# Performance work log

Measured on AMD Instinct MI355X. Metric: run time of the kernel, lower is better.

Reference implementation:

```python
import jax, jax.numpy as jnp
import numpy as np

EMBED = 8   # forced: combine_heads Linear(embed_dim, embed_dim) applied to 8-wire measurement
FFN = 32
B, S = 128, 8192
EPS = 1e-5


def _layernorm(x, g, b):
    m = x.mean(-1, keepdims=True)
    v = ((x - m) ** 2).mean(-1, keepdims=True)
    return (x - m) * jax.lax.rsqrt(v + EPS) * g + b


def setup_inputs() -> dict:
    key = jax.random.key(0)
    ks = jax.random.split(key, 8)

    def lin(k, fi, fo):
        return jax.random.normal(k, (fi, fo), jnp.float32) / np.sqrt(fi).astype(np.float32)

    return dict(
        x=jax.random.normal(ks[0], (B, S, EMBED), jnp.float32),
        Wq=lin(ks[1], EMBED, EMBED), bq=jnp.zeros((EMBED,), jnp.float32),
        theta_attn=jax.random.uniform(ks[2], (EMBED,), jnp.float32, -np.pi, np.pi),
        Wc=lin(ks[3], EMBED, EMBED), bc=jnp.zeros((EMBED,), jnp.float32),
        g1=jnp.ones((EMBED,), jnp.float32), beta1=jnp.zeros((EMBED,), jnp.float32),
        theta_ffn=jax.random.uniform(ks[4], (EMBED,), jnp.float32, -np.pi, np.pi),
        W1=lin(ks[5], EMBED, FFN), b1=jnp.zeros((FFN,), jnp.float32),
        W2=lin(ks[6], FFN, EMBED), b2=jnp.zeros((EMBED,), jnp.float32),
        g2=jnp.ones((EMBED,), jnp.float32), beta2=jnp.zeros((EMBED,), jnp.float32),
    )


def reference(x, Wq, bq, theta_attn, Wc, bc, g1, beta1,
              theta_ffn, W1, b1, W2, b2, g2, beta2):
    # --- MultiHeadAttentionQuantum (eval mode, dropout = identity) ---
    # q_linear; the 8-wire encoder consumes all 8 features of q per token.
    q = x @ Wq + bq                           # [B, S, 8]
    # Circuit per token: RX(q_i) then trainable RX(theta_i) on wire i -> RX(q_i+theta_i),
    # then CNOT ring (0->1,...,6->7, 7->0), then <Z_i>.
    # All-RX product state => basis probs p_i(1)=sin^2(a_i/2); CNOTs permute basis
    # states (prefix-XOR of bits), so analytically:
    #   <Z_k> = prod_{j=0..k} cos(a_j)  for k>=1;   <Z_0> = prod_{j=1..7} cos(a_j)
    ca = jnp.cos(q + theta_attn)              # [B, S, 8]
    z_rest = jnp.cumprod(ca, axis=-1)[..., 1:]
    z0 = jnp.prod(ca[..., 1:], axis=-1, keepdims=True)
    z = jnp.concatenate([z0, z_rest], axis=-1)
    attn_out = z @ Wc + bc                    # combine_heads

    x1 = _layernorm(x + attn_out, g1, beta1)

    # --- FeedForwardQuantum: RX(x_i) then RY(theta_i), no entanglers ->
    #     <Z_i> = cos(theta_i) * cos(x_i)  (product state, per-wire closed form)
    zf = jnp.cos(theta_ffn) * jnp.cos(x1)     # [B, S, 8]
    h = jax.nn.relu(zf @ W1 + b1)             # linear1 -> relu
    ffn_out = h @ W2 + b2                     # linear2

    return _layernorm(x1 + ffn_out, g2, beta2)
```

## Files before the change

### kernel.cpp

```cpp
#include <hip/hip_runtime.h>


#define NTOK   (128 * 8192)
#define NTHREADS 256
#define NBLOCKS  (NTOK / NTHREADS)
#define LN_EPS 1e-5f
#define INV2PI 0.15915494309189535f

typedef __fp16 half2_t __attribute__((ext_vector_type(2)));
typedef __fp16 half8_t __attribute__((ext_vector_type(8)));
typedef float  float4_t __attribute__((ext_vector_type(4)));

union PK  { unsigned u; half2_t h; };
union U4H { uint4 u; half8_t h; half2_t h2[4]; };

__device__ __forceinline__ float fast_cos_rev(float xrev) {
    return __builtin_amdgcn_cosf(xrev);
}
__device__ __forceinline__ float fast_cos(float x) {
    return __builtin_amdgcn_cosf(x * INV2PI);
}
__device__ __forceinline__ float fast_rsqrt(float x) {
    return __builtin_amdgcn_rsqf(x);
}
__device__ __forceinline__ unsigned packh2(float a, float b) {
    PK c; c.h = __builtin_amdgcn_cvt_pkrtz(a, b); return c.u;
}
__device__ __forceinline__ float dot2(half2_t a, unsigned bw, float c) {
    PK b; b.u = bw;
    return __builtin_amdgcn_fdot2(a, b.h, c, false);
}

__global__ void pack_weights(const float* __restrict__ Wq,
                             const float* __restrict__ W1,
                             const float* __restrict__ W2,
                             const float* __restrict__ Wc,
                             const float* __restrict__ bq,
                             const float* __restrict__ tha,
                             const float* __restrict__ thf,
                             unsigned* __restrict__ ws)
{
    int idx = threadIdx.x;
    if (idx < 32) {
        int k = idx >> 2, p = idx & 3;
        ws[idx] = packh2(Wq[(2 * p) * 8 + k] * INV2PI, Wq[(2 * p + 1) * 8 + k] * INV2PI);
    } else if (idx < 64) {
        int i2 = idx - 32;
        int kp = i2 >> 3, j = i2 & 7;
        ws[idx] = packh2(Wc[(2 * kp) * 8 + j], Wc[(2 * kp + 1) * 8 + j]);
    } else if (idx < 72) {
        int k = idx - 64;
        ws[idx] = __float_as_uint((bq[k] + tha[k]) * INV2PI);
    } else if (idx < 80) {
        int j = idx - 72;
        ws[idx] = __float_as_uint(__builtin_amdgcn_cosf(thf[j] * INV2PI));
    } else if (idx >= 128 && idx < 320) {
        int t  = (idx - 128) & 63;
        int tb = (idx - 128) >> 6;
        int n0 = t & 15, q = t >> 4;
        uint4 w = make_uint4(0u, 0u, 0u, 0u);
        unsigned r[4] = {0u, 0u, 0u, 0u};
        if (tb == 0) {
            if (q == 0)
                for (int p = 0; p < 4; ++p)
                    r[p] = packh2(W1[(2 * p) * 32 + n0], W1[(2 * p + 1) * 32 + n0]);
        } else if (tb == 1) {
            if (q == 0)
                for (int p = 0; p < 4; ++p)
                    r[p] = packh2(W1[(2 * p) * 32 + n0 + 16], W1[(2 * p + 1) * 32 + n0 + 16]);
        } else {
            if (n0 < 8)
                for (int p = 0; p < 4; ++p)
                    r[p] = packh2(W2[(8 * q + 2 * p) * 8 + n0], W2[(8 * q + 2 * p + 1) * 8 + n0]);
        }
        w.x = r[0]; w.y = r[1]; w.z = r[2]; w.w = r[3];
        reinterpret_cast<uint4*>(ws)[32 + tb * 64 + t] = w;
    }
}

__global__ __launch_bounds__(NTHREADS, 8)
void qtb_kernel(const float* __restrict__ x,
                const float* __restrict__ bc,
                const float* __restrict__ g1,  const float* __restrict__ be1,
                const float* __restrict__ b1,
                const float* __restrict__ b2,
                const float* __restrict__ g2,  const float* __restrict__ be2,
                const unsigned* __restrict__ wp,
                float* __restrict__ out)
{
    const int tid  = threadIdx.x;
    const int wave = tid >> 6;
    const int lane = tid & 63;
    const int col  = lane & 15;
    const int quad = lane >> 4;
    const int g    = blockIdx.x * NTHREADS + tid;

    const float4* px = reinterpret_cast<const float4*>(x) + (size_t)g * 2;
    float4 xa = px[0];
    float4 xb = px[1];

    const float* qb = reinterpret_cast<const float*>(wp + 64);
    const float* cf = reinterpret_cast<const float*>(wp + 72);

    __shared__ uint4    zbuf[4][64];
    __shared__ unsigned hbuf[4][16 * 20];
    __shared__ float    fbuf[4][64 * 9];

    const uint4* fr = reinterpret_cast<const uint4*>(wp);
    U4H B1a, B1b, B2;
    B1a.u = fr[32 + lane];
    B1b.u = fr[96 + lane];
    B2.u  = fr[160 + lane];
    const float b1a_s = b1[col];
    const float b1b_s = b1[col + 16];
    const float b2_s  = (col < 8) ? b2[col & 7] : 0.f;

    float xv[8];
    half2_t xp[4];
    xv[0] = xa.x; xv[1] = xa.y; xv[2] = xa.z; xv[3] = xa.w;
    xv[4] = xb.x; xv[5] = xb.y; xv[6] = xb.z; xv[7] = xb.w;
    xp[0] = __builtin_amdgcn_cvt_pkrtz(xa.x, xa.y);
    xp[1] = __builtin_amdgcn_cvt_pkrtz(xa.z, xa.w);
    xp[2] = __builtin_amdgcn_cvt_pkrtz(xb.x, xb.y);
    xp[3] = __builtin_amdgcn_cvt_pkrtz(xb.z, xb.w);

    float ca[8];
#pragma unroll
    for (int k = 0; k < 8; ++k) {
        float q = qb[k];
#pragma unroll
        for (int p = 0; p < 4; ++p) q = dot2(xp[p], wp[k * 4 + p], q);
        ca[k] = fast_cos_rev(q);
    }
    float attn[8];
#pragma unroll
    for (int j = 0; j < 8; ++j) attn[j] = bc[j];
    {
        float z[8];
        float cp  = ca[0];
        float cp1 = 1.0f;
#pragma unroll
        for (int k = 1; k < 8; ++k) {
            cp  *= ca[k];
            cp1 *= ca[k];
            z[k] = cp;
        }
        z[0] = cp1;
        half2_t zp[4];
#pragma unroll
        for (int p = 0; p < 4; ++p)
            zp[p] = __builtin_amdgcn_cvt_pkrtz(z[2 * p], z[2 * p + 1]);
#pragma unroll
        for (int p = 0; p < 4; ++p)
#pragma unroll
            for (int j = 0; j < 8; ++j)
                attn[j] = dot2(zp[p], wp[32 + p * 8 + j], attn[j]);
    }

    {
        float y[8];
        float s = 0.f;
#pragma unroll
        for (int j = 0; j < 8; ++j) { y[j] = xv[j] + attn[j]; s += y[j]; }
        float m = s * 0.125f;
        float v = 0.f;
#pragma unroll
        for (int j = 0; j < 8; ++j) { float d = y[j] - m; v += d * d; }
        float r = fast_rsqrt(v * 0.125f + LN_EPS);
        float zf[8];
#pragma unroll
        for (int j = 0; j < 8; ++j) {
            float x1 = (y[j] - m) * r * g1[j] + be1[j];
            xv[j] = x1;
            zf[j] = cf[j] * fast_cos(x1);
        }
        U4H zpk;
#pragma unroll
        for (int p = 0; p < 4; ++p)
            zpk.h2[p] = __builtin_amdgcn_cvt_pkrtz(zf[2 * p], zf[2 * p + 1]);
        zbuf[wave][lane] = zpk.u;
    }

    const unsigned psel = (quad < 2) ? 0x05040100u : 0x07060302u;
#pragma unroll
    for (int grp = 0; grp < 4; ++grp) {
        U4H A1; A1.u = zbuf[wave][grp * 16 + col];
        float4_t c1a = {b1a_s, b1a_s, b1a_s, b1a_s};
        float4_t c1b = {b1b_s, b1b_s, b1b_s, b1b_s};
        float4_t h0 = __builtin_amdgcn_mfma_f32_16x16x32_f16(A1.h, B1a.h, c1a, 0, 0, 0);
        float4_t h1 = __builtin_amdgcn_mfma_f32_16x16x32_f16(A1.h, B1b.h, c1b, 0, 0, 0);
#pragma unroll
        for (int r = 0; r < 4; ++r)
            hbuf[wave][(4 * quad + r) * 20 + col] =
                packh2(fmaxf(h0[r], 0.f), fmaxf(h1[r], 0.f));
        int hb = col * 20 + (quad & 1) * 8;
        uint4 w0 = *reinterpret_cast<const uint4*>(&hbuf[wave][hb]);
        uint4 w1 = *reinterpret_cast<const uint4*>(&hbuf[wave][hb + 4]);
        U4H A2;
        A2.u.x = __builtin_amdgcn_perm(w0.y, w0.x, psel);
        A2.u.y = __builtin_amdgcn_perm(w0.w, w0.z, psel);
        A2.u.z = __builtin_amdgcn_perm(w1.y, w1.x, psel);
        A2.u.w = __builtin_amdgcn_perm(w1.w, w1.z, psel);
        float4_t c2 = {b2_s, b2_s, b2_s, b2_s};
        float4_t f = __builtin_amdgcn_mfma_f32_16x16x32_f16(A2.h, B2.h, c2, 0, 0, 0);
        if (col < 8) {
#pragma unroll
            for (int r = 0; r < 4; ++r)
                fbuf[wave][(grp * 16 + 4 * quad + r) * 9 + col] = f[r];
        }
    }

    {
        float y[8];
        float s = 0.f;
#pragma unroll
        for (int j = 0; j < 8; ++j) {
            y[j] = xv[j] + fbuf[wave][lane * 9 + j];
            s += y[j];
        }
        float m = s * 0.125f;
        float v = 0.f;
#pragma unroll
        for (int j = 0; j < 8; ++j) { float d = y[j] - m; v += d * d; }
        float r = fast_rsqrt(v * 0.125f + LN_EPS);
        float o[8];
#pragma unroll
        for (int j = 0; j < 8; ++j) o[j] = (y[j] - m) * r * g2[j] + be2[j];
        float4* q = reinterpret_cast<float4*>(out) + (size_t)g * 2;
        q[0] = make_float4(o[0], o[1], o[2], o[3]);
        q[1] = make_float4(o[4], o[5], o[6], o[7]);
    }
}

extern "C" void kernel_launch(void* const* d_in, const int* in_sizes, int n_in,
                              void* d_out, int out_size, void* d_ws, size_t ws_size,
                              hipStream_t stream) {
    (void)in_sizes; (void)n_in; (void)ws_size; (void)out_size;
    unsigned* wp = (unsigned*)d_ws;
    pack_weights<<<1, 320, 0, stream>>>(
        (const float*)d_in[1],
        (const float*)d_in[9],
        (const float*)d_in[11],
        (const float*)d_in[4],
        (const float*)d_in[2],
        (const float*)d_in[3],
        (const float*)d_in[8],
        wp);
    qtb_kernel<<<NBLOCKS, NTHREADS, 0, stream>>>(
        (const float*)d_in[0],
        (const float*)d_in[5],
        (const float*)d_in[6],
        (const float*)d_in[7],
        (const float*)d_in[10],
        (const float*)d_in[12],
        (const float*)d_in[13],
        (const float*)d_in[14],
        wp,
        (float*)d_out);
}
```

Baseline: 113.4 us.

## Replace second FFN MFMA with per-thread fdot2 over full hidden row

```diff
diff --git a/kernel.cpp b/kernel.cpp
--- a/kernel.cpp
+++ b/kernel.cpp
@@ -12,7 +12,7 @@
 typedef float  float4_t __attribute__((ext_vector_type(4)));
 
 union PK  { unsigned u; half2_t h; };
-union U4H { uint4 u; half8_t h; half2_t h2[4]; };
+union U4H { uint4 u; half8_t h; half2_t h2[4]; unsigned w[4]; };
 
 __device__ __forceinline__ float fast_cos_rev(float xrev) {
     return __builtin_amdgcn_cosf(xrev);
@@ -54,31 +54,24 @@
     } else if (idx < 80) {
         int j = idx - 72;
         ws[idx] = __float_as_uint(__builtin_amdgcn_cosf(thf[j] * INV2PI));
-    } else if (idx >= 128 && idx < 320) {
-        int t  = (idx - 128) & 63;
-        int tb = (idx - 128) >> 6;
-        int n0 = t & 15, q = t >> 4;
-        uint4 w = make_uint4(0u, 0u, 0u, 0u);
+    } else if (idx < 208) {
+        int i2 = idx - 80;
+        int c = i2 >> 3, j = i2 & 7;
+        ws[idx] = packh2(W2[c * 8 + j], W2[(c + 16) * 8 + j]);
+    } else if (idx >= 256 && idx < 384) {
+        int t  = (idx - 256) & 63;
+        int tb = (idx - 256) >> 6;
+        int n0 = (t & 15) + tb * 16, q = t >> 4;
         unsigned r[4] = {0u, 0u, 0u, 0u};
-        if (tb == 0) {
-            if (q == 0)
-                for (int p = 0; p < 4; ++p)
-                    r[p] = packh2(W1[(2 * p) * 32 + n0], W1[(2 * p + 1) * 32 + n0]);
-        } else if (tb == 1) {
-            if (q == 0)
-                for (int p = 0; p < 4; ++p)
-                    r[p] = packh2(W1[(2 * p) * 32 + n0 + 16], W1[(2 * p + 1) * 32 + n0 + 16]);
-        } else {
-            if (n0 < 8)
-                for (int p = 0; p < 4; ++p)
-                    r[p] = packh2(W2[(8 * q + 2 * p) * 8 + n0], W2[(8 * q + 2 * p + 1) * 8 + n0]);
-        }
-        w.x = r[0]; w.y = r[1]; w.z = r[2]; w.w = r[3];
-        reinterpret_cast<uint4*>(ws)[32 + tb * 64 + t] = w;
-    }
-}
-
-__global__ __launch_bounds__(NTHREADS, 8)
+        if (q == 0)
+            for (int p = 0; p < 4; ++p)
+                r[p] = packh2(W1[(2 * p) * 32 + n0], W1[(2 * p + 1) * 32 + n0]);
+        uint4 w; w.x = r[0]; w.y = r[1]; w.z = r[2]; w.w = r[3];
+        reinterpret_cast<uint4*>(ws)[64 + tb * 64 + t] = w;
+    }
+}
+
+__global__ __launch_bounds__(NTHREADS, 6)
 void qtb_kernel(const float* __restrict__ x,
                 const float* __restrict__ bc,
                 const float* __restrict__ g1,  const float* __restrict__ be1,
@@ -103,17 +96,14 @@
     const float* cf = reinterpret_cast<const float*>(wp + 72);
 
     __shared__ uint4    zbuf[4][64];
-    __shared__ unsigned hbuf[4][16 * 20];
-    __shared__ float    fbuf[4][64 * 9];
+    __shared__ unsigned hbuf[4][64 * 20];
 
     const uint4* fr = reinterpret_cast<const uint4*>(wp);
-    U4H B1a, B1b, B2;
-    B1a.u = fr[32 + lane];
-    B1b.u = fr[96 + lane];
-    B2.u  = fr[160 + lane];
+    U4H B1a, B1b;
+    B1a.u = fr[64 + lane];
+    B1b.u = fr[128 + lane];
     const float b1a_s = b1[col];
     const float b1b_s = b1[col + 16];
-    const float b2_s  = (col < 8) ? b2[col & 7] : 0.f;
 
     float xv[8];
     half2_t xp[4];
@@ -181,7 +171,6 @@
         zbuf[wave][lane] = zpk.u;
     }
 
-    const unsigned psel = (quad < 2) ? 0x05040100u : 0x07060302u;
 #pragma unroll
     for (int grp = 0; grp < 4; ++grp) {
         U4H A1; A1.u = zbuf[wave][grp * 16 + col];
@@ -191,33 +180,33 @@
         float4_t h1 = __builtin_amdgcn_mfma_f32_16x16x32_f16(A1.h, B1b.h, c1b, 0, 0, 0);
 #pragma unroll
         for (int r = 0; r < 4; ++r)
-            hbuf[wave][(4 * quad + r) * 20 + col] =
+            hbuf[wave][(grp * 16 + 4 * quad + r) * 20 + col] =
                 packh2(fmaxf(h0[r], 0.f), fmaxf(h1[r], 0.f));
-        int hb = col * 20 + (quad & 1) * 8;
-        uint4 w0 = *reinterpret_cast<const uint4*>(&hbuf[wave][hb]);
-        uint4 w1 = *reinterpret_cast<const uint4*>(&hbuf[wave][hb + 4]);
-        U4H A2;
-        A2.u.x = __builtin_amdgcn_perm(w0.y, w0.x, psel);
-        A2.u.y = __builtin_amdgcn_perm(w0.w, w0.z, psel);
-        A2.u.z = __builtin_amdgcn_perm(w1.y, w1.x, psel);
-        A2.u.w = __builtin_amdgcn_perm(w1.w, w1.z, psel);
-        float4_t c2 = {b2_s, b2_s, b2_s, b2_s};
-        float4_t f = __builtin_amdgcn_mfma_f32_16x16x32_f16(A2.h, B2.h, c2, 0, 0, 0);
-        if (col < 8) {
-#pragma unroll
-            for (int r = 0; r < 4; ++r)
-                fbuf[wave][(grp * 16 + 4 * quad + r) * 9 + col] = f[r];
-        }
+    }
+
+    U4H hw[4];
+    {
+        const unsigned* hrow = &hbuf[wave][lane * 20];
+#pragma unroll
+        for (int c4 = 0; c4 < 4; ++c4)
+            hw[c4].u = *reinterpret_cast<const uint4*>(hrow + 4 * c4);
+    }
+    float ffn[8];
+#pragma unroll
+    for (int j = 0; j < 8; ++j) ffn[j] = b2[j];
+#pragma unroll
+    for (int c = 0; c < 16; ++c) {
+        half2_t hp = hw[c >> 2].h2[c & 3];
+#pragma unroll
+        for (int j = 0; j < 8; ++j)
+            ffn[j] = dot2(hp, wp[80 + c * 8 + j], ffn[j]);
     }
 
     {
         float y[8];
         float s = 0.f;
 #pragma unroll
-        for (int j = 0; j < 8; ++j) {
-            y[j] = xv[j] + fbuf[wave][lane * 9 + j];
-            s += y[j];
-        }
+        for (int j = 0; j < 8; ++j) { y[j] = xv[j] + ffn[j]; s += y[j]; }
         float m = s * 0.125f;
         float v = 0.f;
 #pragma unroll
@@ -237,7 +226,7 @@
                               hipStream_t stream) {
     (void)in_sizes; (void)n_in; (void)ws_size; (void)out_size;
     unsigned* wp = (unsigned*)d_ws;
-    pack_weights<<<1, 320, 0, stream>>>(
+    pack_weights<<<1, 384, 0, stream>>>(
         (const float*)d_in[1],
         (const float*)d_in[9],
         (const float*)d_in[11],
```

New measurement: 117.9 us. 3.9% more time.

## Use persistent blocks with grid-stride loop and register prefetch of next tokens

Applied to the files above, without the earlier changes.

```diff
diff --git a/kernel.cpp b/kernel.cpp
--- a/kernel.cpp
+++ b/kernel.cpp
@@ -1,9 +1,11 @@
 #include <hip/hip_runtime.h>
 
 
-#define NTOK   (128 * 8192)
+#define NTOK    (128 * 8192)
 #define NTHREADS 256
-#define NBLOCKS  (NTOK / NTHREADS)
+#define PBLOCKS 1024
+#define ITERS   4
+#define CHUNK   (PBLOCKS * NTHREADS)
 #define LN_EPS 1e-5f
 #define INV2PI 0.15915494309189535f
 
@@ -12,7 +14,7 @@
 typedef float  float4_t __attribute__((ext_vector_type(4)));
 
 union PK  { unsigned u; half2_t h; };
-union U4H { uint4 u; half8_t h; half2_t h2[4]; };
+union U4H { uint4 u; half8_t h; half2_t h2[4]; unsigned w[4]; };
 
 __device__ __forceinline__ float fast_cos_rev(float xrev) {
     return __builtin_amdgcn_cosf(xrev);
@@ -58,7 +60,6 @@
         int t  = (idx - 128) & 63;
         int tb = (idx - 128) >> 6;
         int n0 = t & 15, q = t >> 4;
-        uint4 w = make_uint4(0u, 0u, 0u, 0u);
         unsigned r[4] = {0u, 0u, 0u, 0u};
         if (tb == 0) {
             if (q == 0)
@@ -73,12 +74,12 @@
                 for (int p = 0; p < 4; ++p)
                     r[p] = packh2(W2[(8 * q + 2 * p) * 8 + n0], W2[(8 * q + 2 * p + 1) * 8 + n0]);
         }
-        w.x = r[0]; w.y = r[1]; w.z = r[2]; w.w = r[3];
+        uint4 w; w.x = r[0]; w.y = r[1]; w.z = r[2]; w.w = r[3];
         reinterpret_cast<uint4*>(ws)[32 + tb * 64 + t] = w;
     }
 }
 
-__global__ __launch_bounds__(NTHREADS, 8)
+__global__ __launch_bounds__(NTHREADS, 4)
 void qtb_kernel(const float* __restrict__ x,
                 const float* __restrict__ bc,
                 const float* __restrict__ g1,  const float* __restrict__ be1,
@@ -93,18 +94,13 @@
     const int lane = tid & 63;
     const int col  = lane & 15;
     const int quad = lane >> 4;
-    const int g    = blockIdx.x * NTHREADS + tid;
-
-    const float4* px = reinterpret_cast<const float4*>(x) + (size_t)g * 2;
-    float4 xa = px[0];
-    float4 xb = px[1];
 
     const float* qb = reinterpret_cast<const float*>(wp + 64);
     const float* cf = reinterpret_cast<const float*>(wp + 72);
 
     __shared__ uint4    zbuf[4][64];
     __shared__ unsigned hbuf[4][16 * 20];
-    __shared__ float    fbuf[4][64 * 9];
+    __shared__ float    fbuf[4][64 * 10];
 
     const uint4* fr = reinterpret_cast<const uint4*>(wp);
     U4H B1a, B1b, B2;
@@ -114,121 +110,142 @@
     const float b1a_s = b1[col];
     const float b1b_s = b1[col + 16];
     const float b2_s  = (col < 8) ? b2[col & 7] : 0.f;
-
-    float xv[8];
-    half2_t xp[4];
-    xv[0] = xa.x; xv[1] = xa.y; xv[2] = xa.z; xv[3] = xa.w;
-    xv[4] = xb.x; xv[5] = xb.y; xv[6] = xb.z; xv[7] = xb.w;
-    xp[0] = __builtin_amdgcn_cvt_pkrtz(xa.x, xa.y);
-    xp[1] = __builtin_amdgcn_cvt_pkrtz(xa.z, xa.w);
-    xp[2] = __builtin_amdgcn_cvt_pkrtz(xb.x, xb.y);
-    xp[3] = __builtin_amdgcn_cvt_pkrtz(xb.z, xb.w);
-
-    float ca[8];
-#pragma unroll
-    for (int k = 0; k < 8; ++k) {
-        float q = qb[k];
-#pragma unroll
-        for (int p = 0; p < 4; ++p) q = dot2(xp[p], wp[k * 4 + p], q);
-        ca[k] = fast_cos_rev(q);
+    const unsigned psel = (quad < 2) ? 0x05040100u : 0x07060302u;
+
+    size_t g = (size_t)blockIdx.x * NTHREADS + tid;
+    float4 nxa, nxb;
+    {
+        const float4* px = reinterpret_cast<const float4*>(x) + g * 2;
+        nxa = px[0]; nxb = px[1];
     }
-    float attn[8];
-#pragma unroll
-    for (int j = 0; j < 8; ++j) attn[j] = bc[j];
-    {
-        float z[8];
-        float cp  = ca[0];
-        float cp1 = 1.0f;
-#pragma unroll
-        for (int k = 1; k < 8; ++k) {
-            cp  *= ca[k];
-            cp1 *= ca[k];
-            z[k] = cp;
-        }
-        z[0] = cp1;
-        half2_t zp[4];
-#pragma unroll
-        for (int p = 0; p < 4; ++p)
-            zp[p] = __builtin_amdgcn_cvt_pkrtz(z[2 * p], z[2 * p + 1]);
-#pragma unroll
-        for (int p = 0; p < 4; ++p)
-#pragma unroll
-            for (int j = 0; j < 8; ++j)
-                attn[j] = dot2(zp[p], wp[32 + p * 8 + j], attn[j]);
-    }
-
-    {
-        float y[8];
-        float s = 0.f;
-#pragma unroll
-        for (int j = 0; j < 8; ++j) { y[j] = xv[j] + attn[j]; s += y[j]; }
-        float m = s * 0.125f;
-        float v = 0.f;
-#pragma unroll
-        for (int j = 0; j < 8; ++j) { float d = y[j] - m; v += d * d; }
-        float r = fast_rsqrt(v * 0.125f + LN_EPS);
-        float zf[8];
-#pragma unroll
-        for (int j = 0; j < 8; ++j) {
-            float x1 = (y[j] - m) * r * g1[j] + be1[j];
-            xv[j] = x1;
-            zf[j] = cf[j] * fast_cos(x1);
-        }
-        U4H zpk;
-#pragma unroll
-        for (int p = 0; p < 4; ++p)
-            zpk.h2[p] = __builtin_amdgcn_cvt_pkrtz(zf[2 * p], zf[2 * p + 1]);
-        zbuf[wave][lane] = zpk.u;
-    }
-
-    const unsigned psel = (quad < 2) ? 0x05040100u : 0x07060302u;
-#pragma unroll
-    for (int grp = 0; grp < 4; ++grp) {
-        U4H A1; A1.u = zbuf[wave][grp * 16 + col];
-        float4_t c1a = {b1a_s, b1a_s, b1a_s, b1a_s};
-        float4_t c1b = {b1b_s, b1b_s, b1b_s, b1b_s};
-        float4_t h0 = __builtin_amdgcn_mfma_f32_16x16x32_f16(A1.h, B1a.h, c1a, 0, 0, 0);
-        float4_t h1 = __builtin_amdgcn_mfma_f32_16x16x32_f16(A1.h, B1b.h, c1b, 0, 0, 0);
-#pragma unroll
-        for (int r = 0; r < 4; ++r)
-            hbuf[wave][(4 * quad + r) * 20 + col] =
-                packh2(fmaxf(h0[r], 0.f), fmaxf(h1[r], 0.f));
-        int hb = col * 20 + (quad & 1) * 8;
-        uint4 w0 = *reinterpret_cast<const uint4*>(&hbuf[wave][hb]);
-        uint4 w1 = *reinterpret_cast<const uint4*>(&hbuf[wave][hb + 4]);
-        U4H A2;
-        A2.u.x = __builtin_amdgcn_perm(w0.y, w0.x, psel);
-        A2.u.y = __builtin_amdgcn_perm(w0.w, w0.z, psel);
-        A2.u.z = __builtin_amdgcn_perm(w1.y, w1.x, psel);
-        A2.u.w = __builtin_amdgcn_perm(w1.w, w1.z, psel);
-        float4_t c2 = {b2_s, b2_s, b2_s, b2_s};
-        float4_t f = __builtin_amdgcn_mfma_f32_16x16x32_f16(A2.h, B2.h, c2, 0, 0, 0);
-        if (col < 8) {
+
+#pragma unroll 1
+    for (int it = 0; it < ITERS; ++it) {
+        float4 xa = nxa, xb = nxb;
+        const size_t gcur = g;
+        if (it + 1 < ITERS) {
+            g += CHUNK;
+            const float4* px = reinterpret_cast<const float4*>(x) + g * 2;
+            nxa = px[0]; nxb = px[1];
+        }
+
+        float xv[8];
+        half2_t xp[4];
+        xv[0] = xa.x; xv[1] = xa.y; xv[2] = xa.z; xv[3] = xa.w;
+        xv[4] = xb.x; xv[5] = xb.y; xv[6] = xb.z; xv[7] = xb.w;
+        xp[0] = __builtin_amdgcn_cvt_pkrtz(xa.x, xa.y);
+        xp[1] = __builtin_amdgcn_cvt_pkrtz(xa.z, xa.w);
+        xp[2] = __builtin_amdgcn_cvt_pkrtz(xb.x, xb.y);
+        xp[3] = __builtin_amdgcn_cvt_pkrtz(xb.z, xb.w);
+
+        float ca[8];
+#pragma unroll
+        for (int k = 0; k < 8; ++k) {
+            float q = qb[k];
+#pragma unroll
+            for (int p = 0; p < 4; ++p) q = dot2(xp[p], wp[k * 4 + p], q);
+            ca[k] = fast_cos_rev(q);
+        }
+        float attn[8];
+#pragma unroll
+        for (int j = 0; j < 8; ++j) attn[j] = bc[j];
+        {
+            float z[8];
+            float cp  = ca[0];
+            float cp1 = 1.0f;
+#pragma unroll
+            for (int k = 1; k < 8; ++k) {
+                cp  *= ca[k];
+                cp1 *= ca[k];
+                z[k] = cp;
+            }
+            z[0] = cp1;
+            half2_t zp[4];
+#pragma unroll
+            for (int p = 0; p < 4; ++p)
+                zp[p] = __builtin_amdgcn_cvt_pkrtz(z[2 * p], z[2 * p + 1]);
+#pragma unroll
+            for (int p = 0; p < 4; ++p)
+#pragma unroll
+                for (int j = 0; j < 8; ++j)
+                    attn[j] = dot2(zp[p], wp[32 + p * 8 + j], attn[j]);
+        }
+
+        {
+            float y[8];
+            float s = 0.f;
+#pragma unroll
+            for (int j = 0; j < 8; ++j) { y[j] = xv[j] + attn[j]; s += y[j]; }
+            float m = s * 0.125f;
+            float v = 0.f;
+#pragma unroll
+            for (int j = 0; j < 8; ++j) { float d = y[j] - m; v += d * d; }
+            float r = fast_rsqrt(v * 0.125f + LN_EPS);
+            float zf[8];
+#pragma unroll
+            for (int j = 0; j < 8; ++j) {
+                float x1 = (y[j] - m) * r * g1[j] + be1[j];
+                xv[j] = x1;
+                zf[j] = cf[j] * fast_cos(x1);
+            }
+            U4H zpk;
+#pragma unroll
+            for (int p = 0; p < 4; ++p)
+                zpk.h2[p] = __builtin_amdgcn_cvt_pkrtz(zf[2 * p], zf[2 * p + 1]);
+            zbuf[wave][lane] = zpk.u;
+        }
+
+#pragma unroll
+        for (int grp = 0; grp < 4; ++grp) {
+            U4H A1; A1.u = zbuf[wave][grp * 16 + col];
+            float4_t c1a = {b1a_s, b1a_s, b1a_s, b1a_s};
+            float4_t c1b = {b1b_s, b1b_s, b1b_s, b1b_s};
+            float4_t h0 = __builtin_amdgcn_mfma_f32_16x16x32_f16(A1.h, B1a.h, c1a, 0, 0, 0);
+            float4_t h1 = __builtin_amdgcn_mfma_f32_16x16x32_f16(A1.h, B1b.h, c1b, 0, 0, 0);
 #pragma unroll
             for (int r = 0; r < 4; ++r)
-                fbuf[wave][(grp * 16 + 4 * quad + r) * 9 + col] = f[r];
-        }
-    }
-
-    {
-        float y[8];
-        float s = 0.f;
-#pragma unroll
-        for (int j = 0; j < 8; ++j) {
-            y[j] = xv[j] + fbuf[wave][lane * 9 + j];
-            s += y[j];
-        }
-        float m = s * 0.125f;
-        float v = 0.f;
-#pragma unroll
-        for (int j = 0; j < 8; ++j) { float d = y[j] - m; v += d * d; }
-        float r = fast_rsqrt(v * 0.125f + LN_EPS);
-        float o[8];
-#pragma unroll
-        for (int j = 0; j < 8; ++j) o[j] = (y[j] - m) * r * g2[j] + be2[j];
-        float4* q = reinterpret_cast<float4*>(out) + (size_t)g * 2;
-        q[0] = make_float4(o[0], o[1], o[2], o[3]);
-        q[1] = make_float4(o[4], o[5], o[6], o[7]);
+                hbuf[wave][(4 * quad + r) * 20 + col] =
+                    packh2(fmaxf(h0[r], 0.f), fmaxf(h1[r], 0.f));
+            int hb = col * 20 + (quad & 1) * 8;
+            uint4 w0 = *reinterpret_cast<const uint4*>(&hbuf[wave][hb]);
+            uint4 w1 = *reinterpret_cast<const uint4*>(&hbuf[wave][hb + 4]);
+            U4H A2;
+            A2.u.x = __builtin_amdgcn_perm(w0.y, w0.x, psel);
+            A2.u.y = __builtin_amdgcn_perm(w0.w, w0.z, psel);
+            A2.u.z = __builtin_amdgcn_perm(w1.y, w1.x, psel);
+            A2.u.w = __builtin_amdgcn_perm(w1.w, w1.z, psel);
+            float4_t c2 = {b2_s, b2_s, b2_s, b2_s};
+            float4_t f = __builtin_amdgcn_mfma_f32_16x16x32_f16(A2.h, B2.h, c2, 0, 0, 0);
+            if (col < 8) {
+#pragma unroll
+                for (int r = 0; r < 4; ++r)
+                    fbuf[wave][(grp * 16 + 4 * quad + r) * 10 + col] = f[r];
+            }
+        }
+
+        {
+            float y[8];
+            float s = 0.f;
+            const float2* frow = reinterpret_cast<const float2*>(&fbuf[wave][lane * 10]);
+#pragma unroll
+            for (int p = 0; p < 4; ++p) {
+                float2 f2 = frow[p];
+                y[2 * p]     = xv[2 * p]     + f2.x;
+                y[2 * p + 1] = xv[2 * p + 1] + f2.y;
+                s += y[2 * p] + y[2 * p + 1];
+            }
+            float m = s * 0.125f;
+            float v = 0.f;
+#pragma unroll
+            for (int j = 0; j < 8; ++j) { float d = y[j] - m; v += d * d; }
+            float r = fast_rsqrt(v * 0.125f + LN_EPS);
+            float o[8];
+#pragma unroll
+            for (int j = 0; j < 8; ++j) o[j] = (y[j] - m) * r * g2[j] + be2[j];
+            float4* q = reinterpret_cast<float4*>(out) + gcur * 2;
+            q[0] = make_float4(o[0], o[1], o[2], o[3]);
+            q[1] = make_float4(o[4], o[5], o[6], o[7]);
+        }
     }
 }
 
@@ -246,7 +263,7 @@
         (const float*)d_in[3],
         (const float*)d_in[8],
         wp);
-    qtb_kernel<<<NBLOCKS, NTHREADS, 0, stream>>>(
+    qtb_kernel<<<PBLOCKS, NTHREADS, 0, stream>>>(
         (const float*)d_in[0],
         (const float*)d_in[5],
         (const float*)d_in[6],
```

After: 118.5 us. 1.04x slower.

## Process two tokens per thread to amortize weight loads and raise ILP

Applied to the files above, without the earlier changes.

```diff
diff --git a/kernel.cpp b/kernel.cpp
--- a/kernel.cpp
+++ b/kernel.cpp
@@ -1,9 +1,11 @@
 #include <hip/hip_runtime.h>
 
 
-#define NTOK   (128 * 8192)
+#define NTOK    (128 * 8192)
 #define NTHREADS 256
-#define NBLOCKS  (NTOK / NTHREADS)
+#define T 2
+#define NBLOCKS (NTOK / (T * NTHREADS))
+#define TSTRIDE (NTOK / T)
 #define LN_EPS 1e-5f
 #define INV2PI 0.15915494309189535f
 
@@ -12,7 +14,7 @@
 typedef float  float4_t __attribute__((ext_vector_type(4)));
 
 union PK  { unsigned u; half2_t h; };
-union U4H { uint4 u; half8_t h; half2_t h2[4]; };
+union U4H { uint4 u; half8_t h; half2_t h2[4]; unsigned w[4]; };
 
 __device__ __forceinline__ float fast_cos_rev(float xrev) {
     return __builtin_amdgcn_cosf(xrev);
@@ -58,7 +60,6 @@
         int t  = (idx - 128) & 63;
         int tb = (idx - 128) >> 6;
         int n0 = t & 15, q = t >> 4;
-        uint4 w = make_uint4(0u, 0u, 0u, 0u);
         unsigned r[4] = {0u, 0u, 0u, 0u};
         if (tb == 0) {
             if (q == 0)
@@ -73,12 +74,12 @@
                 for (int p = 0; p < 4; ++p)
                     r[p] = packh2(W2[(8 * q + 2 * p) * 8 + n0], W2[(8 * q + 2 * p + 1) * 8 + n0]);
         }
-        w.x = r[0]; w.y = r[1]; w.z = r[2]; w.w = r[3];
+        uint4 w; w.x = r[0]; w.y = r[1]; w.z = r[2]; w.w = r[3];
         reinterpret_cast<uint4*>(ws)[32 + tb * 64 + t] = w;
     }
 }
 
-__global__ __launch_bounds__(NTHREADS, 8)
+__global__ __launch_bounds__(NTHREADS, 4)
 void qtb_kernel(const float* __restrict__ x,
                 const float* __restrict__ bc,
                 const float* __restrict__ g1,  const float* __restrict__ be1,
@@ -93,11 +94,14 @@
     const int lane = tid & 63;
     const int col  = lane & 15;
     const int quad = lane >> 4;
-    const int g    = blockIdx.x * NTHREADS + tid;
-
-    const float4* px = reinterpret_cast<const float4*>(x) + (size_t)g * 2;
-    float4 xa = px[0];
-    float4 xb = px[1];
+    const size_t g = (size_t)blockIdx.x * NTHREADS + tid;
+
+    float4 xa[T], xb[T];
+#pragma unroll
+    for (int s = 0; s < T; ++s) {
+        const float4* px = reinterpret_cast<const float4*>(x) + (g + (size_t)s * TSTRIDE) * 2;
+        xa[s] = px[0]; xb[s] = px[1];
+    }
 
     const float* qb = reinterpret_cast<const float*>(wp + 64);
     const float* cf = reinterpret_cast<const float*>(wp + 72);
@@ -114,35 +118,46 @@
     const float b1a_s = b1[col];
     const float b1b_s = b1[col + 16];
     const float b2_s  = (col < 8) ? b2[col & 7] : 0.f;
-
-    float xv[8];
-    half2_t xp[4];
-    xv[0] = xa.x; xv[1] = xa.y; xv[2] = xa.z; xv[3] = xa.w;
-    xv[4] = xb.x; xv[5] = xb.y; xv[6] = xb.z; xv[7] = xb.w;
-    xp[0] = __builtin_amdgcn_cvt_pkrtz(xa.x, xa.y);
-    xp[1] = __builtin_amdgcn_cvt_pkrtz(xa.z, xa.w);
-    xp[2] = __builtin_amdgcn_cvt_pkrtz(xb.x, xb.y);
-    xp[3] = __builtin_amdgcn_cvt_pkrtz(xb.z, xb.w);
-
-    float ca[8];
+    const unsigned psel = (quad < 2) ? 0x05040100u : 0x07060302u;
+
+    float xv[T][8];
+    half2_t xp[T][4];
+#pragma unroll
+    for (int s = 0; s < T; ++s) {
+        xv[s][0] = xa[s].x; xv[s][1] = xa[s].y; xv[s][2] = xa[s].z; xv[s][3] = xa[s].w;
+        xv[s][4] = xb[s].x; xv[s][5] = xb[s].y; xv[s][6] = xb[s].z; xv[s][7] = xb[s].w;
+        xp[s][0] = __builtin_amdgcn_cvt_pkrtz(xa[s].x, xa[s].y);
+        xp[s][1] = __builtin_amdgcn_cvt_pkrtz(xa[s].z, xa[s].w);
+        xp[s][2] = __builtin_amdgcn_cvt_pkrtz(xb[s].x, xb[s].y);
+        xp[s][3] = __builtin_amdgcn_cvt_pkrtz(xb[s].z, xb[s].w);
+    }
+
+    float ca[T][8];
 #pragma unroll
     for (int k = 0; k < 8; ++k) {
-        float q = qb[k];
-#pragma unroll
-        for (int p = 0; p < 4; ++p) q = dot2(xp[p], wp[k * 4 + p], q);
-        ca[k] = fast_cos_rev(q);
-    }
-    float attn[8];
-#pragma unroll
-    for (int j = 0; j < 8; ++j) attn[j] = bc[j];
-    {
+        const float bqk = qb[k];
+#pragma unroll
+        for (int s = 0; s < T; ++s) {
+            float q = bqk;
+#pragma unroll
+            for (int p = 0; p < 4; ++p) q = dot2(xp[s][p], wp[k * 4 + p], q);
+            ca[s][k] = fast_cos_rev(q);
+        }
+    }
+    float attn[T][8];
+#pragma unroll
+    for (int s = 0; s < T; ++s)
+#pragma unroll
+        for (int j = 0; j < 8; ++j) attn[s][j] = bc[j];
+#pragma unroll
+    for (int s = 0; s < T; ++s) {
         float z[8];
-        float cp  = ca[0];
+        float cp  = ca[s][0];
         float cp1 = 1.0f;
 #pragma unroll
         for (int k = 1; k < 8; ++k) {
-            cp  *= ca[k];
-            cp1 *= ca[k];
+            cp  *= ca[s][k];
+            cp1 *= ca[s][k];
             z[k] = cp;
         }
         z[0] = cp1;
@@ -154,15 +169,17 @@
         for (int p = 0; p < 4; ++p)
 #pragma unroll
             for (int j = 0; j < 8; ++j)
-                attn[j] = dot2(zp[p], wp[32 + p * 8 + j], attn[j]);
-    }
-
-    {
+                attn[s][j] = dot2(zp[p], wp[32 + p * 8 + j], attn[s][j]);
+    }
+
+    U4H zpk[T];
+#pragma unroll
+    for (int s = 0; s < T; ++s) {
         float y[8];
-        float s = 0.f;
-#pragma unroll
-        for (int j = 0; j < 8; ++j) { y[j] = xv[j] + attn[j]; s += y[j]; }
-        float m = s * 0.125f;
+        float ssum = 0.f;
+#pragma unroll
+        for (int j = 0; j < 8; ++j) { y[j] = xv[s][j] + attn[s][j]; ssum += y[j]; }
+        float m = ssum * 0.125f;
         float v = 0.f;
 #pragma unroll
         for (int j = 0; j < 8; ++j) { float d = y[j] - m; v += d * d; }
@@ -171,64 +188,66 @@
 #pragma unroll
         for (int j = 0; j < 8; ++j) {
             float x1 = (y[j] - m) * r * g1[j] + be1[j];
-            xv[j] = x1;
+            xv[s][j] = x1;
             zf[j] = cf[j] * fast_cos(x1);
         }
-        U4H zpk;
 #pragma unroll
         for (int p = 0; p < 4; ++p)
-            zpk.h2[p] = __builtin_amdgcn_cvt_pkrtz(zf[2 * p], zf[2 * p + 1]);
-        zbuf[wave][lane] = zpk.u;
-    }
-
-    const unsigned psel = (quad < 2) ? 0x05040100u : 0x07060302u;
-#pragma unroll
-    for (int grp = 0; grp < 4; ++grp) {
-        U4H A1; A1.u = zbuf[wave][grp * 16 + col];
-        float4_t c1a = {b1a_s, b1a_s, b1a_s, b1a_s};
-        float4_t c1b = {b1b_s, b1b_s, b1b_s, b1b_s};
-        float4_t h0 = __builtin_amdgcn_mfma_f32_16x16x32_f16(A1.h, B1a.h, c1a, 0, 0, 0);
-        float4_t h1 = __builtin_amdgcn_mfma_f32_16x16x32_f16(A1.h, B1b.h, c1b, 0, 0, 0);
-#pragma unroll
-        for (int r = 0; r < 4; ++r)
-            hbuf[wave][(4 * quad + r) * 20 + col] =
-                packh2(fmaxf(h0[r], 0.f), fmaxf(h1[r], 0.f));
-        int hb = col * 20 + (quad & 1) * 8;
-        uint4 w0 = *reinterpret_cast<const uint4*>(&hbuf[wave][hb]);
-        uint4 w1 = *reinterpret_cast<const uint4*>(&hbuf[wave][hb + 4]);
-        U4H A2;
-        A2.u.x = __builtin_amdgcn_perm(w0.y, w0.x, psel);
-        A2.u.y = __builtin_amdgcn_perm(w0.w, w0.z, psel);
-        A2.u.z = __builtin_amdgcn_perm(w1.y, w1.x, psel);
-        A2.u.w = __builtin_amdgcn_perm(w1.w, w1.z, psel);
-        float4_t c2 = {b2_s, b2_s, b2_s, b2_s};
-        float4_t f = __builtin_amdgcn_mfma_f32_16x16x32_f16(A2.h, B2.h, c2, 0, 0, 0);
-        if (col < 8) {
+            zpk[s].h2[p] = __builtin_amdgcn_cvt_pkrtz(zf[2 * p], zf[2 * p + 1]);
+    }
+
+#pragma unroll
+    for (int s = 0; s < T; ++s) {
+        zbuf[wave][lane] = zpk[s].u;
+
+#pragma unroll
+        for (int grp = 0; grp < 4; ++grp) {
+            U4H A1; A1.u = zbuf[wave][grp * 16 + col];
+            float4_t c1a = {b1a_s, b1a_s, b1a_s, b1a_s};
+            float4_t c1b = {b1b_s, b1b_s, b1b_s, b1b_s};
+            float4_t h0 = __builtin_amdgcn_mfma_f32_16x16x32_f16(A1.h, B1a.h, c1a, 0, 0, 0);
+            float4_t h1 = __builtin_amdgcn_mfma_f32_16x16x32_f16(A1.h, B1b.h, c1b, 0, 0, 0);
 #pragma unroll
             for (int r = 0; r < 4; ++r)
-                fbuf[wave][(grp * 16 + 4 * quad + r) * 9 + col] = f[r];
-        }
-    }
-
-    {
-        float y[8];
-        float s = 0.f;
-#pragma unroll
-        for (int j = 0; j < 8; ++j) {
-            y[j] = xv[j] + fbuf[wave][lane * 9 + j];
-            s += y[j];
-        }
-        float m = s * 0.125f;
-        float v = 0.f;
-#pragma unroll
-        for (int j = 0; j < 8; ++j) { float d = y[j] - m; v += d * d; }
-        float r = fast_rsqrt(v * 0.125f + LN_EPS);
-        float o[8];
-#pragma unroll
-        for (int j = 0; j < 8; ++j) o[j] = (y[j] - m) * r * g2[j] + be2[j];
-        float4* q = reinterpret_cast<float4*>(out) + (size_t)g * 2;
-        q[0] = make_float4(o[0], o[1], o[2], o[3]);
-        q[1] = make_float4(o[4], o[5], o[6], o[7]);
+                hbuf[wave][(4 * quad + r) * 20 + col] =
+                    packh2(fmaxf(h0[r], 0.f), fmaxf(h1[r], 0.f));
+            int hb = col * 20 + (quad & 1) * 8;
+            uint4 w0 = *reinterpret_cast<const uint4*>(&hbuf[wave][hb]);
+            uint4 w1 = *reinterpret_cast<const uint4*>(&hbuf[wave][hb + 4]);
+            U4H A2;
+            A2.u.x = __builtin_amdgcn_perm(w0.y, w0.x, psel);
+            A2.u.y = __builtin_amdgcn_perm(w0.w, w0.z, psel);
+            A2.u.z = __builtin_amdgcn_perm(w1.y, w1.x, psel);
+            A2.u.w = __builtin_amdgcn_perm(w1.w, w1.z, psel);
+            float4_t c2 = {b2_s, b2_s, b2_s, b2_s};
+            float4_t f = __builtin_amdgcn_mfma_f32_16x16x32_f16(A2.h, B2.h, c2, 0, 0, 0);
+            if (col < 8) {
+#pragma unroll
+                for (int r = 0; r < 4; ++r)
+                    fbuf[wave][(grp * 16 + 4 * quad + r) * 9 + col] = f[r];
+            }
+        }
+
+        {
+            float y[8];
+            float ssum = 0.f;
+#pragma unroll
+            for (int j = 0; j < 8; ++j) {
+                y[j] = xv[s][j] + fbuf[wave][lane * 9 + j];
+                ssum += y[j];
+            }
+            float m = ssum * 0.125f;
+            float v = 0.f;
+#pragma unroll
+            for (int j = 0; j < 8; ++j) { float d = y[j] - m; v += d * d; }
+            float r = fast_rsqrt(v * 0.125f + LN_EPS);
+            float o[8];
+#pragma unroll
+            for (int j = 0; j < 8; ++j) o[j] = (y[j] - m) * r * g2[j] + be2[j];
+            float4* q = reinterpret_cast<float4*>(out) + (g + (size_t)s * TSTRIDE) * 2;
+            q[0] = make_float4(o[0], o[1], o[2], o[3]);
+            q[1] = make_float4(o[4], o[5], o[6], o[7]);
+        }
     }
 }
 
```

Result: slower. 119.2 us (+5.1%).
